# Kernel optimization log

Hardware: AMD Instinct MI355X
Metric: run time of the kernel (lower is better)

The kernel has to match this reference:

```python
import jax, jax.numpy as jnp
import numpy as np

B, T = 256, 128
EMBED, HIDDEN, VOCAB, FC_IN = 256, 512, 1004, 2048


def setup_inputs() -> dict:
    key = jax.random.key(0)
    ks = jax.random.split(key, 12)
    s = 0.02  # init scale
    return {
        "images": jax.random.normal(ks[0], (B, FC_IN), jnp.float32),   # pooled resnet feats
        "captions": jax.random.normal(ks[1], (B, T, HIDDEN), jnp.float32),
        "W_fc": jax.random.normal(ks[2], (EMBED, FC_IN), jnp.float32) * s,
        "b_fc": jax.random.normal(ks[3], (EMBED,), jnp.float32) * s,
        "W_att": jax.random.normal(ks[4], (EMBED, HIDDEN + EMBED), jnp.float32) * s,
        "b_att": jax.random.normal(ks[5], (EMBED,), jnp.float32) * s,
        "W_ih": jax.random.normal(ks[6], (4 * HIDDEN, 2 * EMBED), jnp.float32) * s,
        "b_ih": jax.random.normal(ks[7], (4 * HIDDEN,), jnp.float32) * s,
        "W_hh": jax.random.normal(ks[8], (4 * HIDDEN, HIDDEN), jnp.float32) * s,
        "b_hh": jax.random.normal(ks[9], (4 * HIDDEN,), jnp.float32) * s,
        "W_out": jax.random.normal(ks[10], (VOCAB, HIDDEN), jnp.float32) * s,
        "b_out": jax.random.normal(ks[11], (VOCAB,), jnp.float32) * s,
    }


def reference(images, captions, W_fc, b_fc, W_att, b_att,
              W_ih, b_ih, W_hh, b_hh, W_out, b_out):
    # encoder fc: pooled resnet features -> embed_size
    feats = images @ W_fc.T + b_fc                      # [B, 256]
    b = feats.shape[0]
    h0 = jnp.zeros((b, HIDDEN), feats.dtype)
    c0 = jnp.zeros((b, HIDDEN), feats.dtype)

    def step(carry, emb_t):
        h, c = carry
        # attention over (features, current caption embed)
        ctx = jnp.concatenate([feats, emb_t], axis=-1) @ W_att.T + b_att   # [B, 256]
        x = jnp.concatenate([feats, ctx], axis=-1)                         # [B, 512]
        gates = x @ W_ih.T + b_ih + h @ W_hh.T + b_hh                      # [B, 2048]
        i, f, g, o = jnp.split(gates, 4, axis=-1)                          # torch gate order
        c = jax.nn.sigmoid(f) * c + jax.nn.sigmoid(i) * jnp.tanh(g)
        h = jax.nn.sigmoid(o) * jnp.tanh(c)
        return (h, c), h

    _, hs = jax.lax.scan(step, (h0, c0), jnp.swapaxes(captions, 0, 1))  # hs: [T, B, 512]
    hiddens = jnp.swapaxes(hs, 0, 1)                                    # [B, T, 512]
    return hiddens @ W_out.T + b_out                                    # [B, T, 1004]
```

## Files before the change

### kernel.cpp

```cpp
#include <hip/hip_runtime.h>

#define Tt  128
#define HID 512

__global__ __launch_bounds__(256)
void gemm_bt(const float* __restrict__ A, const float* __restrict__ Bw,
             const float* __restrict__ bias, const float* __restrict__ C0,
             float* __restrict__ C,
             int M, int N, int K, int lda, int ldb, int ldc, int ldc0, int c0div)
{
    __shared__ float As[16][68];
    __shared__ float Bs[16][68];
    const int n0 = blockIdx.x * 64;
    const int m0 = blockIdx.y * 64;
    const int tid = threadIdx.x;
    const int tx = tid & 15, ty = tid >> 4;
    float acc[4][4];
#pragma unroll
    for (int i = 0; i < 4; i++)
#pragma unroll
        for (int j = 0; j < 4; j++) acc[i][j] = 0.f;

    for (int k0 = 0; k0 < K; k0 += 16) {
#pragma unroll
        for (int i = 0; i < 4; i++) {
            int e = tid + i * 256;
            int m = e >> 4, k = e & 15;
            As[k][m] = A[(size_t)(m0 + m) * lda + (k0 + k)];
        }
#pragma unroll
        for (int i = 0; i < 4; i++) {
            int e = tid + i * 256;
            int n = e >> 4, k = e & 15;
            int gn = n0 + n;
            Bs[k][n] = (gn < N) ? Bw[(size_t)gn * ldb + (k0 + k)] : 0.f;
        }
        __syncthreads();
#pragma unroll
        for (int kk = 0; kk < 16; kk++) {
            float4 av = *(const float4*)&As[kk][ty * 4];
            float4 bv = *(const float4*)&Bs[kk][tx * 4];
            float a[4] = {av.x, av.y, av.z, av.w};
            float b[4] = {bv.x, bv.y, bv.z, bv.w};
#pragma unroll
            for (int i = 0; i < 4; i++)
#pragma unroll
                for (int j = 0; j < 4; j++)
                    acc[i][j] += a[i] * b[j];
        }
        __syncthreads();
    }
#pragma unroll
    for (int i = 0; i < 4; i++) {
        int m = m0 + ty * 4 + i;
        const float* c0row = C0 ? (C0 + (size_t)(m / c0div) * ldc0) : nullptr;
#pragma unroll
        for (int j = 0; j < 4; j++) {
            int n = n0 + tx * 4 + j;
            if (n < N) {
                float v = acc[i][j];
                if (bias)  v += bias[n];
                if (c0row) v += c0row[n];
                C[(size_t)m * ldc + n] = v;
            }
        }
    }
}

__global__ __launch_bounds__(1024, 4)
void lstm_seq(const float* __restrict__ gin, const float* __restrict__ Whh,
              float* __restrict__ hA, float* __restrict__ hB,
              float* __restrict__ hiddens, unsigned int* __restrict__ flags)
{
    __shared__ float4 Ws4[8192];
    __shared__ float4 Hs4[1024];
    const int tid = threadIdx.x;
    const int l   = tid & 63;
    const int w   = tid >> 6;
    const int bt  = blockIdx.x & 7;
    const int jt  = blockIdx.x >> 3;
    const int b0  = bt * 32;
    const int j0  = jt * 16;
    const int jl  = l >> 2;
    const int gl  = l & 3;

    const float4* Whh4 = (const float4*)Whh;
#pragma unroll
    for (int i = 0; i < 8; i++) {
        int row = w + (i & 3) * 16;
        int k4  = (i >> 2) * 64 + l;
        int j_ = row >> 2, g_ = row & 3;
        Ws4[k4 * 64 + (row ^ (k4 & 63))] =
            Whh4[(size_t)(g_ * HID + j0 + j_) * 128 + k4];
    }

    float cr[2] = {0.f, 0.f};
    __syncthreads();

    for (int t = 0; t < Tt; t++) {
        float gp[2];
#pragma unroll
        for (int u = 0; u < 2; u++) {
            int bg = b0 + w * 2 + u;
            gp[u] = gin[((size_t)bg * Tt + t) * 2048 + gl * HID + j0 + jl];
        }
        float acc0 = 0.f, acc1 = 0.f;
        if (t > 0) {
            if (tid == 0) {
                while (__hip_atomic_load(&flags[bt], __ATOMIC_ACQUIRE,
                                         __HIP_MEMORY_SCOPE_AGENT) < 32u * (unsigned)t)
                    __builtin_amdgcn_s_sleep(1);
            }
            __syncthreads();
            const float4* hin4 = (const float4*)(((t - 1) & 1) ? hB : hA);
            for (int c = 0; c < 4; c++) {
                {
                    int kq = tid & 31, bb = tid >> 5;
                    Hs4[bb * 32 + kq] = hin4[(size_t)(b0 + bb) * 128 + c * 32 + kq];
                }
                __syncthreads();
#pragma unroll
                for (int k4 = 0; k4 < 32; k4++) {
                    int kg = c * 32 + k4;
                    float4 wv = Ws4[kg * 64 + (l ^ (kg & 63))];
                    float4 h0 = Hs4[(w * 2 + 0) * 32 + k4];
                    float4 h1 = Hs4[(w * 2 + 1) * 32 + k4];
                    acc0 += wv.x * h0.x + wv.y * h0.y + wv.z * h0.z + wv.w * h0.w;
                    acc1 += wv.x * h1.x + wv.y * h1.y + wv.z * h1.z + wv.w * h1.w;
                }
                __syncthreads();
            }
        }
        float ga0 = acc0 + gp[0];
        float ga1 = acc1 + gp[1];
        int lb = l & ~3;
        float f0 = __shfl(ga0, lb + 1, 64), f1 = __shfl(ga1, lb + 1, 64);
        float g0 = __shfl(ga0, lb + 2, 64), g1 = __shfl(ga1, lb + 2, 64);
        float o0 = __shfl(ga0, lb + 3, 64), o1 = __shfl(ga1, lb + 3, 64);
        float* hw = (t & 1) ? hB : hA;
        if (gl == 0) {
#pragma unroll
            for (int u = 0; u < 2; u++) {
                float gi = u ? ga1 : ga0;
                float gf = u ? f1 : f0;
                float gg = u ? g1 : g0;
                float go = u ? o1 : o0;
                float si = 1.f / (1.f + __expf(-gi));
                float sf = 1.f / (1.f + __expf(-gf));
                float so = 1.f / (1.f + __expf(-go));
                float tg = 1.f - 2.f / (1.f + __expf(2.f * gg));
                float cv = sf * cr[u] + si * tg;
                cr[u] = cv;
                float th = 1.f - 2.f / (1.f + __expf(2.f * cv));
                float hv = so * th;
                int bg = b0 + w * 2 + u, jg = j0 + jl;
                hw[bg * HID + jg] = hv;
                hiddens[((size_t)bg * Tt + t) * HID + jg] = hv;
            }
        }
        __syncthreads();
        if (tid == 0) {
            __threadfence();
            __hip_atomic_fetch_add(&flags[bt], 1u, __ATOMIC_RELEASE,
                                   __HIP_MEMORY_SCOPE_AGENT);
        }
    }
}

extern "C" void kernel_launch(void* const* d_in, const int* in_sizes, int n_in,
                              void* d_out, int out_size, void* d_ws, size_t ws_size,
                              hipStream_t stream)
{
    const float* images = (const float*)d_in[0];
    const float* caps   = (const float*)d_in[1];
    const float* W_fc   = (const float*)d_in[2];
    const float* b_fc   = (const float*)d_in[3];
    const float* W_att  = (const float*)d_in[4];
    const float* b_att  = (const float*)d_in[5];
    const float* W_ih   = (const float*)d_in[6];
    const float* b_ih   = (const float*)d_in[7];
    const float* W_hh   = (const float*)d_in[8];
    const float* b_hh   = (const float*)d_in[9];
    const float* W_out  = (const float*)d_in[10];
    const float* b_out  = (const float*)d_in[11];
    float* out = (float*)d_out;

    float* ws       = (float*)d_ws;
    float* feats    = ws;
    float* att_base = feats + 65536;
    float* gin_base = att_base + 65536;
    float* hA       = gin_base + 524288;
    float* hB       = hA + 131072;
    float* ctx_all  = hB + 131072;
    float* hiddens  = ctx_all + 8388608;
    float* gin_all  = hiddens + 16777216;
    unsigned int* flags = (unsigned int*)(gin_all + 67108864);

    hipMemsetAsync(flags, 0, 8 * sizeof(unsigned int), stream);

    gemm_bt<<<dim3(4, 4), 256, 0, stream>>>(images, W_fc, b_fc, nullptr, feats,
        256, 256, 2048, 2048, 2048, 256, 0, 1);
    gemm_bt<<<dim3(4, 4), 256, 0, stream>>>(feats, W_att, b_att, nullptr, att_base,
        256, 256, 256, 256, 768, 256, 0, 1);
    gemm_bt<<<dim3(32, 4), 256, 0, stream>>>(feats, W_ih, b_ih, nullptr, gin_base,
        256, 2048, 256, 256, 512, 2048, 0, 1);
    gemm_bt<<<dim3(4, 512), 256, 0, stream>>>(caps, W_att + 256, nullptr, att_base, ctx_all,
        32768, 256, 512, 512, 768, 256, 256, Tt);
    gemm_bt<<<dim3(32, 512), 256, 0, stream>>>(ctx_all, W_ih + 256, b_hh, gin_base, gin_all,
        32768, 2048, 256, 256, 512, 2048, 2048, Tt);

    {
        void* args[] = { (void*)&gin_all, (void*)&W_hh, (void*)&hA, (void*)&hB,
                         (void*)&hiddens, (void*)&flags };
        hipLaunchCooperativeKernel((void*)lstm_seq, dim3(256), dim3(1024),
                                   args, 0, stream);
    }

    gemm_bt<<<dim3(16, 512), 256, 0, stream>>>(hiddens, W_out, b_out, nullptr, out,
        32768, 1004, 512, 512, 512, 1004, 0, 1);
}
```

Before: 6.178 ms.

## Keep W_hh slice in registers and reduce LSTM recurrence via wave shuffles

The recurrent kernel now holds each wave's W_hh rows in registers instead of LDS and stages the whole previous h tile into LDS in a single pass, removing the four chunked load/sync rounds per step. Partial dot products are combined with a butterfly shuffle reduce-scatter, so every lane ends up owning one (batch, hidden) element and evaluates the cell update without idle lanes. The input-gate GEMM writes gates interleaved per hidden unit, so each lane reads its four gate preactivations with one float4 load. The kernel drops to 512 threads per block, and the large register arrays raise the risk of spills or low occupancy.

New measurement: 6.111 ms. Within noise of the previous version (-1.1%).

```diff
diff --git a/kernel.cpp b/kernel.cpp
--- a/kernel.cpp
+++ b/kernel.cpp
@@ -7,7 +7,8 @@
 void gemm_bt(const float* __restrict__ A, const float* __restrict__ Bw,
              const float* __restrict__ bias, const float* __restrict__ C0,
              float* __restrict__ C,
-             int M, int N, int K, int lda, int ldb, int ldc, int ldc0, int c0div)
+             int M, int N, int K, int lda, int ldb, int ldc, int ldc0,
+             int c0div, int nperm)
 {
     __shared__ float As[16][68];
     __shared__ float Bs[16][68];
@@ -33,7 +34,8 @@
             int e = tid + i * 256;
             int n = e >> 4, k = e & 15;
             int gn = n0 + n;
-            Bs[k][n] = (gn < N) ? Bw[(size_t)gn * ldb + (k0 + k)] : 0.f;
+            int gr = nperm ? ((gn & 3) * HID + (gn >> 2)) : gn;
+            Bs[k][n] = (gn < N) ? Bw[(size_t)gr * ldb + (k0 + k)] : 0.f;
         }
         __syncthreads();
 #pragma unroll
@@ -59,7 +61,7 @@
             int n = n0 + tx * 4 + j;
             if (n < N) {
                 float v = acc[i][j];
-                if (bias)  v += bias[n];
+                if (bias)  v += bias[nperm ? ((n & 3) * HID + (n >> 2)) : n];
                 if (c0row) v += c0row[n];
                 C[(size_t)m * ldc + n] = v;
             }
@@ -67,13 +69,12 @@
     }
 }
 
-__global__ __launch_bounds__(1024, 4)
+__global__ __launch_bounds__(512, 2)
 void lstm_seq(const float* __restrict__ gin, const float* __restrict__ Whh,
               float* __restrict__ hA, float* __restrict__ hB,
               float* __restrict__ hiddens, unsigned int* __restrict__ flags)
 {
-    __shared__ float4 Ws4[8192];
-    __shared__ float4 Hs4[1024];
+    __shared__ float4 Hs[4096];
     const int tid = threadIdx.x;
     const int l   = tid & 63;
     const int w   = tid >> 6;
@@ -81,30 +82,31 @@
     const int jt  = blockIdx.x >> 3;
     const int b0  = bt * 32;
     const int j0  = jt * 16;
-    const int jl  = l >> 2;
-    const int gl  = l & 3;
-
-    const float4* Whh4 = (const float4*)Whh;
-#pragma unroll
-    for (int i = 0; i < 8; i++) {
-        int row = w + (i & 3) * 16;
-        int k4  = (i >> 2) * 64 + l;
-        int j_ = row >> 2, g_ = row & 3;
-        Ws4[k4 * 64 + (row ^ (k4 & 63))] =
-            Whh4[(size_t)(g_ * HID + j0 + j_) * 128 + k4];
-    }
-
-    float cr[2] = {0.f, 0.f};
-    __syncthreads();
-
-    for (int t = 0; t < Tt; t++) {
-        float gp[2];
-#pragma unroll
-        for (int u = 0; u < 2; u++) {
-            int bg = b0 + w * 2 + u;
-            gp[u] = gin[((size_t)bg * Tt + t) * 2048 + gl * HID + j0 + jl];
-        }
-        float acc0 = 0.f, acc1 = 0.f;
+    const int ot  = l >> 5;
+    const int kc  = l & 31;
+
+    float4 Wr[8][4];
+#pragma unroll
+    for (int r = 0; r < 8; ++r) {
+        int jj = r >> 2, g = r & 3;
+        const float* src = Whh + (size_t)(g * HID + j0 + w * 2 + jj) * HID + kc * 16;
+#pragma unroll
+        for (int q = 0; q < 4; ++q) Wr[r][q] = *(const float4*)(src + q * 4);
+    }
+
+    const int ip  = kc >> 2;
+    const int jjp = (kc >> 1) & 1;
+    const int gH  = kc & 1;
+    const int bp  = b0 + ot * 16 + gH * 8 + ip;
+    const int jp  = j0 + w * 2 + jjp;
+    const size_t hpos = ((size_t)bp * 128 + ((jp >> 2) & 3) * 32 + (jp >> 4)) * 4 + (jp & 3);
+
+    float cr = 0.f;
+
+    for (int t = 0; t < Tt; ++t) {
+        float4 gv = *(const float4*)(gin + ((size_t)bp * Tt + t) * 2048 + jp * 4);
+
+        float rA0 = 0.f, rA1 = 0.f, rB0 = 0.f, rB1 = 0.f;
         if (t > 0) {
             if (tid == 0) {
                 while (__hip_atomic_load(&flags[bt], __ATOMIC_ACQUIRE,
@@ -112,52 +114,82 @@
                     __builtin_amdgcn_s_sleep(1);
             }
             __syncthreads();
-            const float4* hin4 = (const float4*)(((t - 1) & 1) ? hB : hA);
-            for (int c = 0; c < 4; c++) {
-                {
-                    int kq = tid & 31, bb = tid >> 5;
-                    Hs4[bb * 32 + kq] = hin4[(size_t)(b0 + bb) * 128 + c * 32 + kq];
+            {
+                const float4* hin4 =
+                    (const float4*)(((t - 1) & 1) ? hB : hA) + (size_t)b0 * 128;
+                float4 tmp[8];
+#pragma unroll
+                for (int q = 0; q < 8; ++q)
+                    tmp[q] = hin4[(q * 8 + w) * 64 + l];
+#pragma unroll
+                for (int q = 0; q < 8; ++q)
+                    Hs[(q * 8 + w) * 64 + l] = tmp[q];
+            }
+            __syncthreads();
+
+#pragma unroll
+            for (int hb = 0; hb < 2; ++hb) {
+                float P[64];
+#pragma unroll
+                for (int v = 0; v < 64; ++v) P[v] = 0.f;
+#pragma unroll
+                for (int i = 0; i < 8; ++i) {
+                    const float4* hp = &Hs[(ot * 16 + hb * 8 + i) * 128 + kc];
+                    float4 h0 = hp[0], h1 = hp[32], h2 = hp[64], h3 = hp[96];
+#pragma unroll
+                    for (int r = 0; r < 8; ++r) {
+                        P[i * 8 + r] +=
+                            Wr[r][0].x * h0.x + Wr[r][0].y * h0.y + Wr[r][0].z * h0.z + Wr[r][0].w * h0.w +
+                            Wr[r][1].x * h1.x + Wr[r][1].y * h1.y + Wr[r][1].z * h1.z + Wr[r][1].w * h1.w +
+                            Wr[r][2].x * h2.x + Wr[r][2].y * h2.y + Wr[r][2].z * h2.z + Wr[r][2].w * h2.w +
+                            Wr[r][3].x * h3.x + Wr[r][3].y * h3.y + Wr[r][3].z * h3.z + Wr[r][3].w * h3.w;
+                    }
                 }
-                __syncthreads();
-#pragma unroll
-                for (int k4 = 0; k4 < 32; k4++) {
-                    int kg = c * 32 + k4;
-                    float4 wv = Ws4[kg * 64 + (l ^ (kg & 63))];
-                    float4 h0 = Hs4[(w * 2 + 0) * 32 + k4];
-                    float4 h1 = Hs4[(w * 2 + 1) * 32 + k4];
-                    acc0 += wv.x * h0.x + wv.y * h0.y + wv.z * h0.z + wv.w * h0.w;
-                    acc1 += wv.x * h1.x + wv.y * h1.y + wv.z * h1.z + wv.w * h1.w;
+#define RS_STEP(MASK, CNT)                                              \
+                {                                                       \
+                    const int Hh = (CNT) / 2;                           \
+                    const bool hi = (l & (MASK)) != 0;                  \
+                    _Pragma("unroll")                                   \
+                    for (int x = 0; x < Hh; ++x) {                      \
+                        float a = P[x], b2 = P[Hh + x];                 \
+                        float keep = hi ? b2 : a;                       \
+                        float send = hi ? a : b2;                       \
+                        P[x] = keep + __shfl_xor(send, (MASK), 64);     \
+                    }                                                   \
                 }
-                __syncthreads();
-            }
-        }
-        float ga0 = acc0 + gp[0];
-        float ga1 = acc1 + gp[1];
-        int lb = l & ~3;
-        float f0 = __shfl(ga0, lb + 1, 64), f1 = __shfl(ga1, lb + 1, 64);
-        float g0 = __shfl(ga0, lb + 2, 64), g1 = __shfl(ga1, lb + 2, 64);
-        float o0 = __shfl(ga0, lb + 3, 64), o1 = __shfl(ga1, lb + 3, 64);
+                RS_STEP(16, 64)
+                RS_STEP(8, 32)
+                RS_STEP(4, 16)
+                RS_STEP(2, 8)
+                RS_STEP(1, 4)
+#undef RS_STEP
+                if (hb == 0) { rA0 = P[0]; rA1 = P[1]; }
+                else         { rB0 = P[0]; rB1 = P[1]; }
+            }
+        }
+        float own0 = gH ? rB0 : rA0;
+        float own1 = gH ? rB1 : rA1;
+        float snd0 = gH ? rA0 : rB0;
+        float snd1 = gH ? rA1 : rB1;
+        float oth0 = __shfl_xor(snd0, 1, 64);
+        float oth1 = __shfl_xor(snd1, 1, 64);
+        float gi = (gH ? oth0 : own0) + gv.x;
+        float gf = (gH ? oth1 : own1) + gv.y;
+        float gg = (gH ? own0 : oth0) + gv.z;
+        float go = (gH ? own1 : oth1) + gv.w;
+
+        float si = 1.f / (1.f + __expf(-gi));
+        float sf = 1.f / (1.f + __expf(-gf));
+        float so = 1.f / (1.f + __expf(-go));
+        float tg = 1.f - 2.f / (1.f + __expf(2.f * gg));
+        float cv = sf * cr + si * tg;
+        cr = cv;
+        float th = 1.f - 2.f / (1.f + __expf(2.f * cv));
+        float hv = so * th;
+
         float* hw = (t & 1) ? hB : hA;
-        if (gl == 0) {
-#pragma unroll
-            for (int u = 0; u < 2; u++) {
-                float gi = u ? ga1 : ga0;
-                float gf = u ? f1 : f0;
-                float gg = u ? g1 : g0;
-                float go = u ? o1 : o0;
-                float si = 1.f / (1.f + __expf(-gi));
-                float sf = 1.f / (1.f + __expf(-gf));
-                float so = 1.f / (1.f + __expf(-go));
-                float tg = 1.f - 2.f / (1.f + __expf(2.f * gg));
-                float cv = sf * cr[u] + si * tg;
-                cr[u] = cv;
-                float th = 1.f - 2.f / (1.f + __expf(2.f * cv));
-                float hv = so * th;
-                int bg = b0 + w * 2 + u, jg = j0 + jl;
-                hw[bg * HID + jg] = hv;
-                hiddens[((size_t)bg * Tt + t) * HID + jg] = hv;
-            }
-        }
+        hw[hpos] = hv;
+        hiddens[((size_t)bp * Tt + t) * HID + jp] = hv;
         __syncthreads();
         if (tid == 0) {
             __threadfence();
@@ -199,23 +231,23 @@
     hipMemsetAsync(flags, 0, 8 * sizeof(unsigned int), stream);
 
     gemm_bt<<<dim3(4, 4), 256, 0, stream>>>(images, W_fc, b_fc, nullptr, feats,
-        256, 256, 2048, 2048, 2048, 256, 0, 1);
+        256, 256, 2048, 2048, 2048, 256, 0, 1, 0);
     gemm_bt<<<dim3(4, 4), 256, 0, stream>>>(feats, W_att, b_att, nullptr, att_base,
-        256, 256, 256, 256, 768, 256, 0, 1);
+        256, 256, 256, 256, 768, 256, 0, 1, 0);
     gemm_bt<<<dim3(32, 4), 256, 0, stream>>>(feats, W_ih, b_ih, nullptr, gin_base,
-        256, 2048, 256, 256, 512, 2048, 0, 1);
+        256, 2048, 256, 256, 512, 2048, 0, 1, 1);
     gemm_bt<<<dim3(4, 512), 256, 0, stream>>>(caps, W_att + 256, nullptr, att_base, ctx_all,
-        32768, 256, 512, 512, 768, 256, 256, Tt);
+        32768, 256, 512, 512, 768, 256, 256, Tt, 0);
     gemm_bt<<<dim3(32, 512), 256, 0, stream>>>(ctx_all, W_ih + 256, b_hh, gin_base, gin_all,
-        32768, 2048, 256, 256, 512, 2048, 2048, Tt);
+        32768, 2048, 256, 256, 512, 2048, 2048, Tt, 1);
 
     {
         void* args[] = { (void*)&gin_all, (void*)&W_hh, (void*)&hA, (void*)&hB,
                          (void*)&hiddens, (void*)&flags };
-        hipLaunchCooperativeKernel((void*)lstm_seq, dim3(256), dim3(1024),
+        hipLaunchCooperativeKernel((void*)lstm_seq, dim3(256), dim3(512),
                                    args, 0, stream);
     }
 
     gemm_bt<<<dim3(16, 512), 256, 0, stream>>>(hiddens, W_out, b_out, nullptr, out,
-        32768, 1004, 512, 512, 512, 1004, 0, 1);
+        32768, 1004, 512, 512, 512, 1004, 0, 1, 0);
 }
```
